# Performance work log

Measured on AMD Instinct MI355X. Metric: run time of the kernel, lower is better.

The kernel has to match this reference:

```python
import jax, jax.numpy as jnp
import numpy as np

N = 2_000_000   # query points
B = 4           # scene batches
F = 16          # keyframes
R = 96          # grid resolution per axis


def setup_inputs() -> dict:
    key = jax.random.key(0)
    k1, k2, k3, k4 = jax.random.split(key, 4)
    pts = jax.random.uniform(k1, (N, 3), jnp.float32, -1.0, 1.0)   # in [-1,1]
    ts = jax.random.uniform(k2, (N,), jnp.float32, 0.0, 1.0)
    occ_grid = jax.random.uniform(k3, (B * F, R, R, R), jnp.float32)  # flat (batch*frame) occupancy
    ts_keyframes = jnp.linspace(0.0, 1.0, F, dtype=jnp.float32)       # sorted keyframe times
    bidx = jax.random.randint(k4, (N,), 0, B, jnp.int32)
    return {"pts": pts, "ts": ts, "occ_grid": occ_grid,
            "ts_keyframes": ts_keyframes, "bidx": bidx}


def reference(pts, ts, occ_grid, ts_keyframes, bidx):
    """cur_batch__query_occupancy: nearest-keyframe lookup + flat occ-grid gather."""
    res = occ_grid.shape[-1]
    n_frames = ts_keyframes.shape[0]
    # gidx = ((pts / 2 + 0.5) * resolution).long().clamp(0, R-1)
    gidx = jnp.clip(jnp.floor((pts * 0.5 + 0.5) * res).astype(jnp.int32), 0, res - 1)
    # torch_consecutive_nearest1d: nearest index in sorted ts_keyframes
    ins = jnp.searchsorted(ts_keyframes, ts)
    lo = jnp.clip(ins - 1, 0, n_frames - 1)
    hi = jnp.clip(ins, 0, n_frames - 1)
    fidx = jnp.where(jnp.abs(ts_keyframes[hi] - ts) < jnp.abs(ts - ts_keyframes[lo]), hi, lo)
    flat_bidx = bidx.astype(jnp.int32) * n_frames + fidx
    # occ_grid[flat_bidx, gx, gy, gz]
    return occ_grid[flat_bidx, gidx[:, 0], gidx[:, 1], gidx[:, 2]]
```

## Files before the change

### kernel.cpp

```cpp
#include <hip/hip_runtime.h>


__global__ __launch_bounds__(256) void occ_query_kernel(
    const float* __restrict__ pts,
    const float* __restrict__ ts,
    const float* __restrict__ occ,
    const float* __restrict__ kf,
    const int*   __restrict__ bidx,
    float*       __restrict__ out,
    int n)
{
    constexpr int R = 96;
    constexpr int F = 16;
    constexpr int R3 = R * R * R;

    float k[F];
#pragma unroll
    for (int j = 0; j < F; ++j) k[j] = kf[j];

    const int stride = gridDim.x * blockDim.x;
    for (int i = blockIdx.x * blockDim.x + threadIdx.x; i < n; i += stride) {
        const float px = pts[3 * i + 0];
        const float py = pts[3 * i + 1];
        const float pz = pts[3 * i + 2];
        const float t  = ts[i];
        const int   b  = bidx[i];

        int gx = (int)floorf((px * 0.5f + 0.5f) * (float)R);
        int gy = (int)floorf((py * 0.5f + 0.5f) * (float)R);
        int gz = (int)floorf((pz * 0.5f + 0.5f) * (float)R);
        gx = min(max(gx, 0), R - 1);
        gy = min(max(gy, 0), R - 1);
        gz = min(max(gz, 0), R - 1);

        int ins = 0;
#pragma unroll
        for (int j = 0; j < F; ++j) ins += (k[j] < t) ? 1 : 0;
        int lo = min(max(ins - 1, 0), F - 1);
        int hi = min(ins, F - 1);
        const int f = (fabsf(k[hi] - t) < fabsf(t - k[lo])) ? hi : lo;

        const int flat = (b * F + f) * R3 + (gx * R + gy) * R + gz;
        out[i] = occ[flat];
    }
}

extern "C" void kernel_launch(void* const* d_in, const int* in_sizes, int n_in,
                              void* d_out, int out_size, void* d_ws, size_t ws_size,
                              hipStream_t stream)
{
    const float* pts  = (const float*)d_in[0];
    const float* ts   = (const float*)d_in[1];
    const float* occ  = (const float*)d_in[2];
    const float* kf   = (const float*)d_in[3];
    const int*   bidx = (const int*)d_in[4];
    float* out = (float*)d_out;

    const int n = in_sizes[1];

    int blocks = (n + 255) / 256;
    if (blocks > 2048) blocks = 2048;

    occ_query_kernel<<<blocks, 256, 0, stream>>>(pts, ts, occ, kf, bidx, out, n);
}
```

Before: 327.3 us.

## Process four points per thread with vectorized nontemporal loads and stores

Each thread now handles four consecutive queries, loading pts, ts and bidx as 128-bit vectors with nontemporal hints and writing four outputs in one vector store. The grid-stride loop with a 2048-block cap is replaced by one thread per four points. This targets the strided 12-byte pts accesses and per-element load overhead, and keeps four random occ gathers in flight per thread. The gathers themselves stay random and likely dominate, so the benefit depends on how much of the time streaming inputs account for.

```diff
diff --git a/kernel.cpp b/kernel.cpp
--- a/kernel.cpp
+++ b/kernel.cpp
@@ -1,7 +1,10 @@
 #include <hip/hip_runtime.h>
 
 
-__global__ __launch_bounds__(256) void occ_query_kernel(
+typedef float f32x4 __attribute__((ext_vector_type(4)));
+typedef int   i32x4 __attribute__((ext_vector_type(4)));
+
+__global__ __launch_bounds__(256) void occ_query4_kernel(
     const float* __restrict__ pts,
     const float* __restrict__ ts,
     const float* __restrict__ occ,
@@ -10,38 +13,82 @@
     float*       __restrict__ out,
     int n)
 {
-    constexpr int R = 96;
-    constexpr int F = 16;
+    constexpr int R  = 96;
+    constexpr int F  = 16;
     constexpr int R3 = R * R * R;
 
     float k[F];
 #pragma unroll
     for (int j = 0; j < F; ++j) k[j] = kf[j];
 
-    const int stride = gridDim.x * blockDim.x;
-    for (int i = blockIdx.x * blockDim.x + threadIdx.x; i < n; i += stride) {
-        const float px = pts[3 * i + 0];
-        const float py = pts[3 * i + 1];
-        const float pz = pts[3 * i + 2];
-        const float t  = ts[i];
-        const int   b  = bidx[i];
+    const int tid = blockIdx.x * blockDim.x + threadIdx.x;
+    const int i0  = tid * 4;
+    if (i0 >= n) return;
 
-        int gx = (int)floorf((px * 0.5f + 0.5f) * (float)R);
-        int gy = (int)floorf((py * 0.5f + 0.5f) * (float)R);
-        int gz = (int)floorf((pz * 0.5f + 0.5f) * (float)R);
-        gx = min(max(gx, 0), R - 1);
-        gy = min(max(gy, 0), R - 1);
-        gz = min(max(gz, 0), R - 1);
+    if (i0 + 4 <= n) {
+        const f32x4* p4 = (const f32x4*)pts;
+        const f32x4 a  = __builtin_nontemporal_load(&p4[tid * 3 + 0]);
+        const f32x4 b  = __builtin_nontemporal_load(&p4[tid * 3 + 1]);
+        const f32x4 c  = __builtin_nontemporal_load(&p4[tid * 3 + 2]);
+        const f32x4 t4 = __builtin_nontemporal_load(&((const f32x4*)ts)[tid]);
+        const i32x4 b4 = __builtin_nontemporal_load(&((const i32x4*)bidx)[tid]);
 
-        int ins = 0;
+        const float px[4] = {a.x, a.w, b.z, c.y};
+        const float py[4] = {a.y, b.x, b.w, c.z};
+        const float pz[4] = {a.z, b.y, c.x, c.w};
+        const float tt[4] = {t4.x, t4.y, t4.z, t4.w};
+        const int   bb[4] = {b4.x, b4.y, b4.z, b4.w};
+
+        int flat[4];
 #pragma unroll
-        for (int j = 0; j < F; ++j) ins += (k[j] < t) ? 1 : 0;
-        int lo = min(max(ins - 1, 0), F - 1);
-        int hi = min(ins, F - 1);
-        const int f = (fabsf(k[hi] - t) < fabsf(t - k[lo])) ? hi : lo;
+        for (int q = 0; q < 4; ++q) {
+            int gx = (int)floorf((px[q] * 0.5f + 0.5f) * (float)R);
+            int gy = (int)floorf((py[q] * 0.5f + 0.5f) * (float)R);
+            int gz = (int)floorf((pz[q] * 0.5f + 0.5f) * (float)R);
+            gx = min(max(gx, 0), R - 1);
+            gy = min(max(gy, 0), R - 1);
+            gz = min(max(gz, 0), R - 1);
 
-        const int flat = (b * F + f) * R3 + (gx * R + gy) * R + gz;
-        out[i] = occ[flat];
+            int ins = 0;
+#pragma unroll
+            for (int j = 0; j < F; ++j) ins += (k[j] < tt[q]) ? 1 : 0;
+            const int lo = min(max(ins - 1, 0), F - 1);
+            const int hi = min(ins, F - 1);
+            const int f  = (fabsf(k[hi] - tt[q]) < fabsf(tt[q] - k[lo])) ? hi : lo;
+
+            flat[q] = (bb[q] * F + f) * R3 + (gx * R + gy) * R + gz;
+        }
+
+        f32x4 r;
+        r.x = occ[flat[0]];
+        r.y = occ[flat[1]];
+        r.z = occ[flat[2]];
+        r.w = occ[flat[3]];
+        __builtin_nontemporal_store(r, &((f32x4*)out)[tid]);
+    } else {
+        for (int i = i0; i < n; ++i) {
+            const float px = pts[3 * i + 0];
+            const float py = pts[3 * i + 1];
+            const float pz = pts[3 * i + 2];
+            const float t  = ts[i];
+            const int   bq = bidx[i];
+
+            int gx = (int)floorf((px * 0.5f + 0.5f) * (float)R);
+            int gy = (int)floorf((py * 0.5f + 0.5f) * (float)R);
+            int gz = (int)floorf((pz * 0.5f + 0.5f) * (float)R);
+            gx = min(max(gx, 0), R - 1);
+            gy = min(max(gy, 0), R - 1);
+            gz = min(max(gz, 0), R - 1);
+
+            int ins = 0;
+#pragma unroll
+            for (int j = 0; j < F; ++j) ins += (k[j] < t) ? 1 : 0;
+            const int lo = min(max(ins - 1, 0), F - 1);
+            const int hi = min(ins, F - 1);
+            const int f  = (fabsf(k[hi] - t) < fabsf(t - k[lo])) ? hi : lo;
+
+            out[i] = occ[(bq * F + f) * R3 + (gx * R + gy) * R + gz];
+        }
     }
 }
 
@@ -57,9 +104,8 @@
     float* out = (float*)d_out;
 
     const int n = in_sizes[1];
+    const int nthreads = (n + 3) / 4;
+    const int blocks = (nthreads + 255) / 256;
 
-    int blocks = (n + 255) / 256;
-    if (blocks > 2048) blocks = 2048;
-
-    occ_query_kernel<<<blocks, 256, 0, stream>>>(pts, ts, occ, kf, bidx, out, n);
+    occ_query4_kernel<<<blocks, 256, 0, stream>>>(pts, ts, occ, kf, bidx, out, n);
 }
```

New measurement: 322.8 us. No clear change (-1.4%).
